# Performance work log

Hardware: AMD Instinct MI355X
Metric: run time of the kernel (lower is better)

Reference implementation:

```python
import jax, jax.numpy as jnp
import numpy as np

# DeformConv (RegSeg): offset conv + mask conv (sigmoid) + modulated deformable conv v2
STRIDE = 1
PAD = 1
DIL = 1
G = 1          # deformable_groups
KH, KW = 3, 3


def _conv(x, w, b):
    # standard NCHW conv, stride/pad/dilation of the module
    y = jax.lax.conv_general_dilated(
        x, w, window_strides=(STRIDE, STRIDE),
        padding=((PAD, PAD), (PAD, PAD)), rhs_dilation=(DIL, DIL),
        dimension_numbers=("NCHW", "OIHW", "NCHW"))
    return y + b[None, :, None, None]


def _deform_conv2d(x, offset, mask, w, b):
    # torchvision DeformConv2d (modulated, v2) semantics
    B, C, H, W = x.shape
    O = w.shape[0]
    K = KH * KW
    Ho = (H + 2 * PAD - DIL * (KH - 1) - 1) // STRIDE + 1
    Wo = (W + 2 * PAD - DIL * (KW - 1) - 1) // STRIDE + 1
    Cg = C // G

    # base sampling grid: p0 + p_k
    ky = jnp.repeat(jnp.arange(KH), KW) * DIL            # [K]
    kx = jnp.tile(jnp.arange(KW), KH) * DIL              # [K]
    oy = jnp.arange(Ho) * STRIDE - PAD                   # [Ho]
    ox = jnp.arange(Wo) * STRIDE - PAD                   # [Wo]
    base_y = (ky[:, None, None] + oy[None, :, None]).astype(x.dtype)  # [K,Ho,1]
    base_x = (kx[:, None, None] + ox[None, None, :]).astype(x.dtype)  # [K,1,Wo]

    off = offset.reshape(B, G, K, 2, Ho, Wo)             # channel layout: g, k, (dy,dx)
    py = base_y[None, None] + off[:, :, :, 0]            # [B,G,K,Ho,Wo]
    px = base_x[None, None] + off[:, :, :, 1]
    m = mask.reshape(B, G, K, Ho, Wo)

    imgf = x.reshape(B * G, Cg, H * W)
    y0 = jnp.floor(py).astype(jnp.int32)
    x0 = jnp.floor(px).astype(jnp.int32)
    ly = py - y0.astype(x.dtype)
    lx = px - x0.astype(x.dtype)

    def corner(iy, ix, wgt):
        # zero-padded bilinear corner: out-of-bounds corners contribute 0
        valid = (iy >= 0) & (iy < H) & (ix >= 0) & (ix < W)
        idx = (jnp.clip(iy, 0, H - 1) * W + jnp.clip(ix, 0, W - 1)).reshape(B * G, -1)
        g = jax.vmap(lambda im, ii: im[:, ii])(imgf, idx)            # [B*G,Cg,K*Ho*Wo]
        g = g.reshape(B, G, Cg, K, Ho, Wo)
        return g * (wgt * valid.astype(x.dtype))[:, :, None]          # [B,G,Cg,K,Ho,Wo]

    val = (corner(y0,     x0,     (1 - ly) * (1 - lx))
         + corner(y0,     x0 + 1, (1 - ly) * lx)
         + corner(y0 + 1, x0,     ly * (1 - lx))
         + corner(y0 + 1, x0 + 1, ly * lx))
    val = val * m[:, :, None]                                         # modulation

    wr = w.reshape(O, G, Cg, K)
    out = jnp.einsum("bgckpq,ogck->bopq", val, wr) + b[None, :, None, None]
    return out


def setup_inputs() -> dict:
    key = jax.random.key(0)
    ks = jax.random.split(key, 8)
    B, C, H, W, O = 4, 128, 96, 96, 128
    K = KH * KW
    fan = 1.0 / np.sqrt(C * K)
    return {
        "x":        jax.random.normal(ks[0], (B, C, H, W), jnp.float32),
        "x2":       jax.random.normal(ks[1], (B, C, H, W), jnp.float32),
        "offset_w": jax.random.normal(ks[2], (2 * G * K, C, KH, KW), jnp.float32) * 0.01,
        "offset_b": jax.random.normal(ks[3], (2 * G * K,), jnp.float32) * 0.01,
        "mask_w":   jax.random.normal(ks[4], (G * K, C, KH, KW), jnp.float32) * 0.05,
        "mask_b":   jnp.zeros((G * K,), jnp.float32),
        "deform_w": jax.random.normal(ks[5], (O, C, KH, KW), jnp.float32) * fan,
        "deform_b": jax.random.normal(ks[6], (O,), jnp.float32) * fan,
    }


def reference(x, x2, offset_w, offset_b, mask_w, mask_b, deform_w, deform_b):
    offset = _conv(x2, offset_w, offset_b)
    mask = jax.nn.sigmoid(_conv(x2, mask_w, mask_b))
    return _deform_conv2d(x, offset, mask, deform_w, deform_b)
```

## Files before the change

### kernel.cpp

```cpp
#include <hip/hip_runtime.h>

#define CIN   128
#define HH    96
#define WW    96
#define OUTC  128
#define HWSZ  9216
#define KK    9
#define KTOT  1152

typedef __bf16 bf16x8 __attribute__((ext_vector_type(8)));
typedef float  f32x4  __attribute__((ext_vector_type(4)));

__device__ __forceinline__ unsigned short f2bf(float f) {
  unsigned u = __builtin_bit_cast(unsigned, f);
  u += 0x7fffu + ((u >> 16) & 1u);
  return (unsigned short)(u >> 16);
}
__device__ __forceinline__ float bf2f_lo(unsigned w) {
  unsigned u = w << 16;
  return __builtin_bit_cast(float, u);
}
__device__ __forceinline__ float bf2f_hi(unsigned w) {
  unsigned u = w & 0xffff0000u;
  return __builtin_bit_cast(float, u);
}
__device__ __forceinline__ unsigned pack_bf(float v0, float v1) {
  unsigned u0 = __builtin_bit_cast(unsigned, v0) + 0x8000u;
  unsigned u1 = __builtin_bit_cast(unsigned, v1) + 0x8000u;
  return __builtin_amdgcn_perm(u1, u0, 0x07060302u);
}

#define WT2B_O 147456
#define BIAS_O 184320
#define XN_O   184384
#define X2N_O  (184384 + 4718592)

__global__ __launch_bounds__(256) void prep_all(
    const float* __restrict__ x, const float* __restrict__ x2,
    const float* __restrict__ offw, const float* __restrict__ maskw,
    const float* __restrict__ defw, const float* __restrict__ offb,
    const float* __restrict__ maskb, void* __restrict__ wsv) {
  int bid = blockIdx.x;
  int t = threadIdx.x;
  if (bid < 1152) {
    __shared__ unsigned short tile[64][136];
    int tsel = bid / 576;
    int rem = bid - tsel * 576;
    int b = rem / 144;
    int hw0 = (rem % 144) * 64;
    const float* src = tsel ? x2 : x;
    unsigned short* dst = (unsigned short*)wsv + (tsel ? X2N_O : XN_O);
    unsigned* tw = (unsigned*)&tile[0][0];
    int c2  = t & 15;
    int px4 = t >> 4;
#pragma unroll
    for (int pass = 0; pass < 4; ++pass) {
      int c = pass * 32 + c2 * 2;
      const float* r0 = src + ((size_t)(b * CIN + c)) * HWSZ + hw0 + px4 * 4;
      float4 f0 = *(const float4*)r0;
      float4 f1 = *(const float4*)(r0 + HWSZ);
      int wb = pass * 16 + c2;
      tw[(px4 * 4 + 0) * 68 + wb] = pack_bf(f0.x, f1.x);
      tw[(px4 * 4 + 1) * 68 + wb] = pack_bf(f0.y, f1.y);
      tw[(px4 * 4 + 2) * 68 + wb] = pack_bf(f0.z, f1.z);
      tw[(px4 * 4 + 3) * 68 + wb] = pack_bf(f0.w, f1.w);
    }
    __syncthreads();
    unsigned* drow = (unsigned*)(dst + ((size_t)(b * HWSZ + hw0)) * 128);
    int w4 = t & 15, pxr = t >> 4;
#pragma unroll
    for (int pass = 0; pass < 4; ++pass) {
      int px = pass * 16 + pxr;
      uint4 v = *(const uint4*)&tw[px * 68 + w4 * 4];
      *(uint4*)&drow[(size_t)px * 64 + w4 * 4] = v;
    }
    return;
  }
  unsigned short* wtb  = (unsigned short*)wsv;
  unsigned short* wt2b = wtb + WT2B_O;
  float* bias32 = (float*)(wtb + BIAS_O);
  int idx = (bid - 1152) * 256 + t;
  if (idx < OUTC * KTOT) {
    int o = idx / KTOT, r = idx - o * KTOT;
    int c = r / KK, tap = r - c * KK;
    wtb[o * KTOT + tap * 128 + c] = f2bf(defw[idx]);
  } else if (idx < OUTC * KTOT + 32 * KTOT) {
    int j = idx - OUTC * KTOT;
    int oc = j / KTOT, r = j - oc * KTOT;
    int c = r / KK, tap = r - c * KK;
    float v = 0.f;
    if (oc < 18)      v = offw[j];
    else if (oc < 27) v = maskw[j - 18 * KTOT];
    wt2b[oc * KTOT + tap * 128 + c] = f2bf(v);
  } else if (idx < OUTC * KTOT + 32 * KTOT + 32) {
    int j = idx - OUTC * KTOT - 32 * KTOT;
    float v = 0.f;
    if (j < 18) v = offb[j]; else if (j < 27) v = maskb[j - 18];
    bias32[j] = v;
  }
}

__global__ __launch_bounds__(256, 3) void fused(
    const float* __restrict__ defb, const void* __restrict__ wsv,
    float* __restrict__ out) {
  const unsigned short* wtb  = (const unsigned short*)wsv;
  const unsigned short* wt2b = wtb + WT2B_O;
  const float* bias32 = (const float*)(wtb + BIAS_O);
  const unsigned short* xn  = wtb + XN_O;
  const unsigned short* x2n = wtb + X2N_O;

  __shared__ unsigned bw[64 * 68];
  __shared__ unsigned short val[64][136];
  __shared__ float om[32][68];
  __shared__ unsigned sidxw[KK * 4 * 64];

  int t = threadIdx.x;
  int w = t >> 6;
  int l15 = t & 15, quad = (t >> 4) & 3;
  int rb = blockIdx.x;
  int bid = (rb & 7) * 72 + (rb >> 3);
  int b = bid / 144;
  int pblk = (bid % 144) * 64;

  int phg[4], pwg[4];
#pragma unroll
  for (int G = 0; G < 4; ++G) {
    int p = pblk + w * 16 + G * 4 + quad;
    phg[G] = p / WW;
    pwg[G] = p - phg[G] * WW;
  }

  f32x4 oa0 = {0.f, 0.f, 0.f, 0.f};
  f32x4 oa1 = {0.f, 0.f, 0.f, 0.f};
  const unsigned short* x2nb = x2n + ((size_t)b * HWSZ) * 128;
  for (int tap = 0; tap < KK; ++tap) {
    int ky = tap / 3 - 1, kx = tap % 3 - 1;
    uint4 vG[4];
#pragma unroll
    for (int G = 0; G < 4; ++G) {
      int y = phg[G] + ky, xx = pwg[G] + kx;
      bool ok = ((unsigned)y < HH) && ((unsigned)xx < WW);
      int pos = ok ? (y * WW + xx) : 0;
      uint4 v = *(const uint4*)(x2nb + ((size_t)pos << 7) + l15 * 8);
      vG[G] = ok ? v : make_uint4(0u, 0u, 0u, 0u);
    }
#pragma unroll
    for (int j = 0; j < 2; ++j) {
      int cc = t + 256 * j;
      int row = cc >> 4, c16 = cc & 15;
      *(uint4*)&bw[row * 68 + c16 * 4] =
          *(const uint4*)(wt2b + (size_t)row * KTOT + tap * 128 + c16 * 8);
    }
#pragma unroll
    for (int G = 0; G < 4; ++G)
      *(uint4*)&val[w * 16 + G * 4 + quad][l15 * 8] = vG[G];
    __syncthreads();
#pragma unroll
    for (int ks = 0; ks < 4; ++ks) {
      bf16x8 af = *(const bf16x8*)&val[w * 16 + l15][ks * 32 + quad * 8];
      bf16x8 b0 = *(const bf16x8*)&bw[(size_t)l15 * 68 + ks * 16 + quad * 4];
      bf16x8 b1 = *(const bf16x8*)&bw[(size_t)(l15 + 16) * 68 + ks * 16 + quad * 4];
      oa0 = __builtin_amdgcn_mfma_f32_16x16x32_bf16(af, b0, oa0, 0, 0, 0);
      oa1 = __builtin_amdgcn_mfma_f32_16x16x32_bf16(af, b1, oa1, 0, 0, 0);
    }
    __syncthreads();
  }
#pragma unroll
  for (int nt = 0; nt < 2; ++nt) {
    f32x4 a = nt ? oa1 : oa0;
    int oc = nt * 16 + l15;
    float bia = bias32[oc];
#pragma unroll
    for (int r = 0; r < 4; ++r)
      om[oc][w * 16 + quad * 4 + r] = a[r] + bia;
  }
  __syncthreads();

  for (int e = t; e < KK * 64; e += 256) {
    int tap = e >> 6, pp = e & 63;
    int gp2 = pblk + pp;
    int h = gp2 / WW, ww_ = gp2 % WW;
    float dy = om[2 * tap][pp], dx = om[2 * tap + 1][pp];
    float mr = om[18 + tap][pp];
    float m = 1.f / (1.f + __expf(-mr));
    float py  = (float)(h + tap / 3 - 1) + dy;
    float pxx = (float)(ww_ + tap % 3 - 1) + dx;
    float y0f = floorf(py), x0f = floorf(pxx);
    int y0 = (int)y0f, x0 = (int)x0f;
    float ly = py - y0f, lx = pxx - x0f;
    int y1 = y0 + 1, x1 = x0 + 1;
    bool vy0 = (unsigned)y0 < HH, vy1 = (unsigned)y1 < HH;
    bool vx0 = (unsigned)x0 < WW, vx1 = (unsigned)x1 < WW;
    int cy0 = min(max(y0, 0), HH - 1), cy1 = min(max(y1, 0), HH - 1);
    int cx0 = min(max(x0, 0), WW - 1), cx1 = min(max(x1, 0), WW - 1);
    unsigned i00 = cy0 * WW + cx0, i01 = cy0 * WW + cx1;
    unsigned i10 = cy1 * WW + cx0, i11 = cy1 * WW + cx1;
    float w00 = (vy0 && vx0) ? m * (1.f - ly) * (1.f - lx) : 0.f;
    float w01 = (vy0 && vx1) ? m * (1.f - ly) * lx         : 0.f;
    float w10 = (vy1 && vx0) ? m * ly * (1.f - lx)         : 0.f;
    float w11 = (vy1 && vx1) ? m * ly * lx                 : 0.f;
    sidxw[(tap * 4 + 0) * 64 + pp] = i00 | ((unsigned)f2bf(w00) << 16);
    sidxw[(tap * 4 + 1) * 64 + pp] = i01 | ((unsigned)f2bf(w01) << 16);
    sidxw[(tap * 4 + 2) * 64 + pp] = i10 | ((unsigned)f2bf(w10) << 16);
    sidxw[(tap * 4 + 3) * 64 + pp] = i11 | ((unsigned)f2bf(w11) << 16);
  }
  __syncthreads();

  f32x4 acc[8];
#pragma unroll
  for (int nt = 0; nt < 8; ++nt) acc[nt] = (f32x4){0.f, 0.f, 0.f, 0.f};
  const unsigned short* xnb = xn + ((size_t)b * HWSZ) * 128;

  for (int tap = 0; tap < KK; ++tap) {
    unsigned sw[4][4];
#pragma unroll
    for (int cr = 0; cr < 4; ++cr)
#pragma unroll
      for (int G = 0; G < 4; ++G)
        sw[cr][G] = sidxw[(tap * 4 + cr) * 64 + w * 16 + G * 4 + quad];
    uint4 v[4][4];
#pragma unroll
    for (int G = 0; G < 4; ++G)
#pragma unroll
      for (int cr = 0; cr < 4; ++cr)
        v[cr][G] = *(const uint4*)(xnb + ((size_t)(sw[cr][G] & 0xffffu) << 7) + l15 * 8);
#pragma unroll
    for (int G = 0; G < 4; ++G) {
      float f[8];
#pragma unroll
      for (int j = 0; j < 8; ++j) f[j] = 0.f;
#pragma unroll
      for (int cr = 0; cr < 4; ++cr) {
        float wc = bf2f_hi(sw[cr][G]);
        const unsigned* a = (const unsigned*)&v[cr][G];
#pragma unroll
        for (int j = 0; j < 4; ++j) {
          f[2 * j]     += wc * bf2f_lo(a[j]);
          f[2 * j + 1] += wc * bf2f_hi(a[j]);
        }
      }
      unsigned od[4];
#pragma unroll
      for (int j = 0; j < 4; ++j) od[j] = pack_bf(f[2 * j], f[2 * j + 1]);
      *(uint4*)&val[w * 16 + G * 4 + quad][l15 * 8] =
          make_uint4(od[0], od[1], od[2], od[3]);
    }
#pragma unroll
    for (int j = 0; j < 4; ++j) {
      int cc = t + 256 * j;
      int row = cc >> 4, c16 = cc & 15;
      *(uint4*)&bw[row * 68 + c16 * 4] =
          *(const uint4*)(wtb + (size_t)row * KTOT + tap * 128 + c16 * 8);
    }
    __syncthreads();
    bf16x8 af[4];
#pragma unroll
    for (int ks = 0; ks < 4; ++ks)
      af[ks] = *(const bf16x8*)&val[w * 16 + l15][ks * 32 + quad * 8];
#pragma unroll
    for (int ks = 0; ks < 4; ++ks)
#pragma unroll
      for (int nt = 0; nt < 4; ++nt) {
        bf16x8 bb = *(const bf16x8*)&bw[(size_t)(nt * 16 + l15) * 68 + ks * 16 + quad * 4];
        acc[nt] = __builtin_amdgcn_mfma_f32_16x16x32_bf16(af[ks], bb, acc[nt], 0, 0, 0);
      }
    __syncthreads();
#pragma unroll
    for (int j = 0; j < 4; ++j) {
      int cc = t + 256 * j;
      int row = cc >> 4, c16 = cc & 15;
      *(uint4*)&bw[row * 68 + c16 * 4] =
          *(const uint4*)(wtb + (size_t)(64 + row) * KTOT + tap * 128 + c16 * 8);
    }
    __syncthreads();
#pragma unroll
    for (int ks = 0; ks < 4; ++ks)
#pragma unroll
      for (int nt = 0; nt < 4; ++nt) {
        bf16x8 bb = *(const bf16x8*)&bw[(size_t)(nt * 16 + l15) * 68 + ks * 16 + quad * 4];
        acc[4 + nt] = __builtin_amdgcn_mfma_f32_16x16x32_bf16(af[ks], bb, acc[4 + nt], 0, 0, 0);
      }
    __syncthreads();
  }

  for (int r = 0; r < 4; ++r) {
    f32x4 a0 = acc[2 * r], a1 = acc[2 * r + 1];
    float db0 = defb[r * 32 + l15];
    float db1 = defb[r * 32 + 16 + l15];
    if (r) __syncthreads();
#pragma unroll
    for (int reg = 0; reg < 4; ++reg) {
      om[l15]     [w * 16 + quad * 4 + reg] = a0[reg] + db0;
      om[16 + l15][w * 16 + quad * 4 + reg] = a1[reg] + db1;
    }
    __syncthreads();
    int row = t >> 4;
    int col4 = (t & 15) * 4;
#pragma unroll
    for (int hrow = 0; hrow < 2; ++hrow) {
      int rr = row + hrow * 16;
      float4 vv = *(float4*)&om[rr][col4];
      *(float4*)&out[((size_t)b * OUTC + r * 32 + rr) * HWSZ + pblk + col4] = vv;
    }
  }
}

extern "C" void kernel_launch(void* const* d_in, const int* in_sizes, int n_in,
                              void* d_out, int out_size, void* d_ws, size_t ws_size,
                              hipStream_t stream) {
  const float* x     = (const float*)d_in[0];
  const float* x2    = (const float*)d_in[1];
  const float* offw  = (const float*)d_in[2];
  const float* offb  = (const float*)d_in[3];
  const float* maskw = (const float*)d_in[4];
  const float* maskb = (const float*)d_in[5];
  const float* defw  = (const float*)d_in[6];
  const float* defb  = (const float*)d_in[7];
  float* out = (float*)d_out;

  hipLaunchKernelGGL(prep_all, dim3(1873), dim3(256), 0, stream,
                     x, x2, offw, maskw, defw, offb, maskb, d_ws);
  hipLaunchKernelGGL(fused, dim3(576), dim3(256), 0, stream, defb, d_ws, out);
}
```

Measured before the change: 147.0 us.

## Halve pixel tile per block and split K across wave pairs with LDS reduction

Each block now handles 32 output pixels instead of 64, and the grid doubles to 1152 blocks. The four waves are arranged as two M-halves times two K-halves: each wave gathers and interpolates half the pixels and runs MFMAs over half the channel range. The partial sums are then reduced through shared memory before the epilogue. Shared memory per block shrinks and launch bounds rise to 4 blocks per CU, aiming for more parallelism and latency hiding. The cost is that the deformable weight tiles are reloaded twice as often per output pixel, and the kernel gains an extra reduction and barrier.

```diff
diff --git a/kernel.cpp b/kernel.cpp
--- a/kernel.cpp
+++ b/kernel.cpp
@@ -100,7 +100,7 @@
   }
 }
 
-__global__ __launch_bounds__(256, 3) void fused(
+__global__ __launch_bounds__(256, 4) void fused(
     const float* __restrict__ defb, const void* __restrict__ wsv,
     float* __restrict__ out) {
   const unsigned short* wtb  = (const unsigned short*)wsv;
@@ -110,24 +110,25 @@
   const unsigned short* x2n = wtb + X2N_O;
 
   __shared__ unsigned bw[64 * 68];
-  __shared__ unsigned short val[64][136];
-  __shared__ float om[32][68];
-  __shared__ unsigned sidxw[KK * 4 * 64];
+  __shared__ unsigned short val[32][136];
+  __shared__ float om[32][36];
+  __shared__ unsigned sidxw[KK * 4 * 32];
 
   int t = threadIdx.x;
   int w = t >> 6;
+  int m = w & 1, k2 = w >> 1;
   int l15 = t & 15, quad = (t >> 4) & 3;
   int rb = blockIdx.x;
-  int bid = (rb & 7) * 72 + (rb >> 3);
-  int b = bid / 144;
-  int pblk = (bid % 144) * 64;
-
-  int phg[4], pwg[4];
-#pragma unroll
-  for (int G = 0; G < 4; ++G) {
-    int p = pblk + w * 16 + G * 4 + quad;
-    phg[G] = p / WW;
-    pwg[G] = p - phg[G] * WW;
+  int bid = (rb & 7) * 144 + (rb >> 3);
+  int b = bid / 288;
+  int base = (bid % 288) * 32;
+
+  int phg[2], pwg[2];
+#pragma unroll
+  for (int gi = 0; gi < 2; ++gi) {
+    int p = base + m * 16 + (2 * k2 + gi) * 4 + quad;
+    phg[gi] = p / WW;
+    pwg[gi] = p - phg[gi] * WW;
   }
 
   f32x4 oa0 = {0.f, 0.f, 0.f, 0.f};
@@ -135,14 +136,14 @@
   const unsigned short* x2nb = x2n + ((size_t)b * HWSZ) * 128;
   for (int tap = 0; tap < KK; ++tap) {
     int ky = tap / 3 - 1, kx = tap % 3 - 1;
-    uint4 vG[4];
-#pragma unroll
-    for (int G = 0; G < 4; ++G) {
-      int y = phg[G] + ky, xx = pwg[G] + kx;
+    uint4 vG[2];
+#pragma unroll
+    for (int gi = 0; gi < 2; ++gi) {
+      int y = phg[gi] + ky, xx = pwg[gi] + kx;
       bool ok = ((unsigned)y < HH) && ((unsigned)xx < WW);
       int pos = ok ? (y * WW + xx) : 0;
       uint4 v = *(const uint4*)(x2nb + ((size_t)pos << 7) + l15 * 8);
-      vG[G] = ok ? v : make_uint4(0u, 0u, 0u, 0u);
+      vG[gi] = ok ? v : make_uint4(0u, 0u, 0u, 0u);
     }
 #pragma unroll
     for (int j = 0; j < 2; ++j) {
@@ -152,12 +153,12 @@
           *(const uint4*)(wt2b + (size_t)row * KTOT + tap * 128 + c16 * 8);
     }
 #pragma unroll
-    for (int G = 0; G < 4; ++G)
-      *(uint4*)&val[w * 16 + G * 4 + quad][l15 * 8] = vG[G];
+    for (int gi = 0; gi < 2; ++gi)
+      *(uint4*)&val[m * 16 + (2 * k2 + gi) * 4 + quad][l15 * 8] = vG[gi];
     __syncthreads();
 #pragma unroll
     for (int ks = 0; ks < 4; ++ks) {
-      bf16x8 af = *(const bf16x8*)&val[w * 16 + l15][ks * 32 + quad * 8];
+      bf16x8 af = *(const bf16x8*)&val[m * 16 + l15][ks * 32 + quad * 8];
       bf16x8 b0 = *(const bf16x8*)&bw[(size_t)l15 * 68 + ks * 16 + quad * 4];
       bf16x8 b1 = *(const bf16x8*)&bw[(size_t)(l15 + 16) * 68 + ks * 16 + quad * 4];
       oa0 = __builtin_amdgcn_mfma_f32_16x16x32_bf16(af, b0, oa0, 0, 0, 0);
@@ -172,17 +173,17 @@
     float bia = bias32[oc];
 #pragma unroll
     for (int r = 0; r < 4; ++r)
-      om[oc][w * 16 + quad * 4 + r] = a[r] + bia;
+      om[oc][m * 16 + quad * 4 + r] = a[r] + bia;
   }
   __syncthreads();
 
-  for (int e = t; e < KK * 64; e += 256) {
-    int tap = e >> 6, pp = e & 63;
-    int gp2 = pblk + pp;
+  for (int e = t; e < KK * 32; e += 256) {
+    int tap = e >> 5, pp = e & 31;
+    int gp2 = base + pp;
     int h = gp2 / WW, ww_ = gp2 % WW;
     float dy = om[2 * tap][pp], dx = om[2 * tap + 1][pp];
     float mr = om[18 + tap][pp];
-    float m = 1.f / (1.f + __expf(-mr));
+    float mm = 1.f / (1.f + __expf(-mr));
     float py  = (float)(h + tap / 3 - 1) + dy;
     float pxx = (float)(ww_ + tap % 3 - 1) + dx;
     float y0f = floorf(py), x0f = floorf(pxx);
@@ -195,14 +196,14 @@
     int cx0 = min(max(x0, 0), WW - 1), cx1 = min(max(x1, 0), WW - 1);
     unsigned i00 = cy0 * WW + cx0, i01 = cy0 * WW + cx1;
     unsigned i10 = cy1 * WW + cx0, i11 = cy1 * WW + cx1;
-    float w00 = (vy0 && vx0) ? m * (1.f - ly) * (1.f - lx) : 0.f;
-    float w01 = (vy0 && vx1) ? m * (1.f - ly) * lx         : 0.f;
-    float w10 = (vy1 && vx0) ? m * ly * (1.f - lx)         : 0.f;
-    float w11 = (vy1 && vx1) ? m * ly * lx                 : 0.f;
-    sidxw[(tap * 4 + 0) * 64 + pp] = i00 | ((unsigned)f2bf(w00) << 16);
-    sidxw[(tap * 4 + 1) * 64 + pp] = i01 | ((unsigned)f2bf(w01) << 16);
-    sidxw[(tap * 4 + 2) * 64 + pp] = i10 | ((unsigned)f2bf(w10) << 16);
-    sidxw[(tap * 4 + 3) * 64 + pp] = i11 | ((unsigned)f2bf(w11) << 16);
+    float w00 = (vy0 && vx0) ? mm * (1.f - ly) * (1.f - lx) : 0.f;
+    float w01 = (vy0 && vx1) ? mm * (1.f - ly) * lx         : 0.f;
+    float w10 = (vy1 && vx0) ? mm * ly * (1.f - lx)         : 0.f;
+    float w11 = (vy1 && vx1) ? mm * ly * lx                 : 0.f;
+    sidxw[(tap * 4 + 0) * 32 + pp] = i00 | ((unsigned)f2bf(w00) << 16);
+    sidxw[(tap * 4 + 1) * 32 + pp] = i01 | ((unsigned)f2bf(w01) << 16);
+    sidxw[(tap * 4 + 2) * 32 + pp] = i10 | ((unsigned)f2bf(w10) << 16);
+    sidxw[(tap * 4 + 3) * 32 + pp] = i11 | ((unsigned)f2bf(w11) << 16);
   }
   __syncthreads();
 
@@ -212,27 +213,27 @@
   const unsigned short* xnb = xn + ((size_t)b * HWSZ) * 128;
 
   for (int tap = 0; tap < KK; ++tap) {
-    unsigned sw[4][4];
+    unsigned sw[4][2];
 #pragma unroll
     for (int cr = 0; cr < 4; ++cr)
 #pragma unroll
-      for (int G = 0; G < 4; ++G)
-        sw[cr][G] = sidxw[(tap * 4 + cr) * 64 + w * 16 + G * 4 + quad];
-    uint4 v[4][4];
-#pragma unroll
-    for (int G = 0; G < 4; ++G)
+      for (int gi = 0; gi < 2; ++gi)
+        sw[cr][gi] = sidxw[(tap * 4 + cr) * 32 + m * 16 + (2 * k2 + gi) * 4 + quad];
+    uint4 v[4][2];
+#pragma unroll
+    for (int gi = 0; gi < 2; ++gi)
 #pragma unroll
       for (int cr = 0; cr < 4; ++cr)
-        v[cr][G] = *(const uint4*)(xnb + ((size_t)(sw[cr][G] & 0xffffu) << 7) + l15 * 8);
-#pragma unroll
-    for (int G = 0; G < 4; ++G) {
+        v[cr][gi] = *(const uint4*)(xnb + ((size_t)(sw[cr][gi] & 0xffffu) << 7) + l15 * 8);
+#pragma unroll
+    for (int gi = 0; gi < 2; ++gi) {
       float f[8];
 #pragma unroll
       for (int j = 0; j < 8; ++j) f[j] = 0.f;
 #pragma unroll
       for (int cr = 0; cr < 4; ++cr) {
-        float wc = bf2f_hi(sw[cr][G]);
-        const unsigned* a = (const unsigned*)&v[cr][G];
+        float wc = bf2f_hi(sw[cr][gi]);
+        const unsigned* a = (const unsigned*)&v[cr][gi];
 #pragma unroll
         for (int j = 0; j < 4; ++j) {
           f[2 * j]     += wc * bf2f_lo(a[j]);
@@ -242,7 +243,7 @@
       unsigned od[4];
 #pragma unroll
       for (int j = 0; j < 4; ++j) od[j] = pack_bf(f[2 * j], f[2 * j + 1]);
-      *(uint4*)&val[w * 16 + G * 4 + quad][l15 * 8] =
+      *(uint4*)&val[m * 16 + (2 * k2 + gi) * 4 + quad][l15 * 8] =
           make_uint4(od[0], od[1], od[2], od[3]);
     }
 #pragma unroll
@@ -253,16 +254,16 @@
           *(const uint4*)(wtb + (size_t)row * KTOT + tap * 128 + c16 * 8);
     }
     __syncthreads();
-    bf16x8 af[4];
-#pragma unroll
-    for (int ks = 0; ks < 4; ++ks)
-      af[ks] = *(const bf16x8*)&val[w * 16 + l15][ks * 32 + quad * 8];
-#pragma unroll
-    for (int ks = 0; ks < 4; ++ks)
+    bf16x8 af[2];
+#pragma unroll
+    for (int i = 0; i < 2; ++i)
+      af[i] = *(const bf16x8*)&val[m * 16 + l15][(2 * k2 + i) * 32 + quad * 8];
+#pragma unroll
+    for (int i = 0; i < 2; ++i)
 #pragma unroll
       for (int nt = 0; nt < 4; ++nt) {
-        bf16x8 bb = *(const bf16x8*)&bw[(size_t)(nt * 16 + l15) * 68 + ks * 16 + quad * 4];
-        acc[nt] = __builtin_amdgcn_mfma_f32_16x16x32_bf16(af[ks], bb, acc[nt], 0, 0, 0);
+        bf16x8 bb = *(const bf16x8*)&bw[(size_t)(nt * 16 + l15) * 68 + (2 * k2 + i) * 16 + quad * 4];
+        acc[nt] = __builtin_amdgcn_mfma_f32_16x16x32_bf16(af[i], bb, acc[nt], 0, 0, 0);
       }
     __syncthreads();
 #pragma unroll
@@ -274,34 +275,52 @@
     }
     __syncthreads();
 #pragma unroll
-    for (int ks = 0; ks < 4; ++ks)
+    for (int i = 0; i < 2; ++i)
 #pragma unroll
       for (int nt = 0; nt < 4; ++nt) {
-        bf16x8 bb = *(const bf16x8*)&bw[(size_t)(nt * 16 + l15) * 68 + ks * 16 + quad * 4];
-        acc[4 + nt] = __builtin_amdgcn_mfma_f32_16x16x32_bf16(af[ks], bb, acc[4 + nt], 0, 0, 0);
+        bf16x8 bb = *(const bf16x8*)&bw[(size_t)(nt * 16 + l15) * 68 + (2 * k2 + i) * 16 + quad * 4];
+        acc[4 + nt] = __builtin_amdgcn_mfma_f32_16x16x32_bf16(af[i], bb, acc[4 + nt], 0, 0, 0);
       }
     __syncthreads();
   }
 
+  {
+    float* xch = (float*)bw;
+    int lane = t & 63;
+    if (k2 == 1) {
+#pragma unroll
+      for (int nt = 0; nt < 8; ++nt)
+#pragma unroll
+        for (int r = 0; r < 4; ++r)
+          xch[(nt * 4 + r) * 128 + m * 64 + lane] = acc[nt][r];
+    }
+    __syncthreads();
+    if (k2 == 0) {
+#pragma unroll
+      for (int nt = 0; nt < 8; ++nt)
+#pragma unroll
+        for (int r = 0; r < 4; ++r)
+          acc[nt][r] += xch[(nt * 4 + r) * 128 + m * 64 + lane];
+    }
+  }
+
   for (int r = 0; r < 4; ++r) {
-    f32x4 a0 = acc[2 * r], a1 = acc[2 * r + 1];
-    float db0 = defb[r * 32 + l15];
-    float db1 = defb[r * 32 + 16 + l15];
     if (r) __syncthreads();
-#pragma unroll
-    for (int reg = 0; reg < 4; ++reg) {
-      om[l15]     [w * 16 + quad * 4 + reg] = a0[reg] + db0;
-      om[16 + l15][w * 16 + quad * 4 + reg] = a1[reg] + db1;
-    }
-    __syncthreads();
-    int row = t >> 4;
-    int col4 = (t & 15) * 4;
-#pragma unroll
-    for (int hrow = 0; hrow < 2; ++hrow) {
-      int rr = row + hrow * 16;
-      float4 vv = *(float4*)&om[rr][col4];
-      *(float4*)&out[((size_t)b * OUTC + r * 32 + rr) * HWSZ + pblk + col4] = vv;
-    }
+    if (k2 == 0) {
+      f32x4 a0 = acc[2 * r], a1 = acc[2 * r + 1];
+      float db0 = defb[r * 32 + l15];
+      float db1 = defb[r * 32 + 16 + l15];
+#pragma unroll
+      for (int reg = 0; reg < 4; ++reg) {
+        om[l15]     [m * 16 + quad * 4 + reg] = a0[reg] + db0;
+        om[16 + l15][m * 16 + quad * 4 + reg] = a1[reg] + db1;
+      }
+    }
+    __syncthreads();
+    int row = t >> 3;
+    int col4 = (t & 7) * 4;
+    float4 vv = *(float4*)&om[row][col4];
+    *(float4*)&out[((size_t)b * OUTC + r * 32 + row) * HWSZ + base + col4] = vv;
   }
 }
 
@@ -320,5 +339,5 @@
 
   hipLaunchKernelGGL(prep_all, dim3(1873), dim3(256), 0, stream,
                      x, x2, offw, maskw, defw, offb, maskb, d_ws);
-  hipLaunchKernelGGL(fused, dim3(576), dim3(256), 0, stream, defb, d_ws, out);
-}
+  hipLaunchKernelGGL(fused, dim3(1152), dim3(256), 0, stream, defb, d_ws, out);
+}
```

Result: slower. 176.4 us (+20.0%).
